# Kernel optimization log

Hardware: AMD Instinct MI355X
Metric: run time of the kernel (lower is better)

The kernel has to match this reference:

```python
import jax, jax.numpy as jnp
import numpy as np

B, N, K, H = 1, 8192, 32, 16
FIBER_IN = (16, 8)
NC_OUT = {'00': 8, '10': 8, '01': 4, '11': 4}
# (pair_key, nc_in, nc_out, num_freq) with num_freq = 2*min(di,do)+1
PAIRS = (('00', 16, 8, 1), ('10', 8, 8, 1), ('01', 16, 4, 1), ('11', 8, 4, 3))


def _silu(x):
    return x * jax.nn.sigmoid(x)


def _ln(x, g):
    mu = x.mean(-1, keepdims=True)
    var = ((x - mu) ** 2).mean(-1, keepdims=True)
    return (x - mu) * jax.lax.rsqrt(var + 1e-5) * g


def _radial(feat, p):
    # Linear -> SiLU -> LayerNorm -> Linear -> SiLU -> LayerNorm -> Linear
    w1, b1, g1, w2, b2, g2, w3, b3 = p
    h = _ln(_silu(feat @ w1 + b1), g1)
    h = _ln(_silu(h @ w2 + b2), g2)
    return h @ w3 + b3


def _lin(x, w):
    # degreewise Linear: einsum('... d m, d e -> ... e m')
    return jnp.einsum('bndm,de->bnem', x, w)


def _forward(x0, x1, rel_dist, bases, w_xi, w_xj, rps, w_out, w_si, nbr_idx, nbr_mask):
    inp = {0: x0, 1: x1}
    xi = {d: _lin(inp[d], w_xi[d]) for d in (0, 1)}
    xj = {d: _lin(inp[d], w_xj[d]) for d in (0, 1)}
    gather = jax.vmap(lambda f, i: f[i])  # per batch: [n,d,m],[n,k] -> [n,k,d,m]
    mask = nbr_mask.astype(x0.dtype)  # [b,n,k]
    denom = jnp.maximum(mask.sum(-1), 1.0)[..., None, None]  # [b,n,1,1]
    b, n, k = nbr_idx.shape
    outs = {}
    for do in (0, 1):
        chunks = []
        for di in (0, 1):
            pkey = str(di) + str(do)
            ci, co = FIBER_IN[di], NC_OUT[pkey]
            nf = 2 * min(di, do) + 1
            xg = gather(xj[di], nbr_idx) + xi[di][:, :, None]  # [b,n,k,ci,mi]
            R = _radial(rel_dist, rps[pkey]).reshape(b, n, k, co, ci, nf)
            Bt = bases[pkey].reshape(b, n, k, 2 * do + 1, 2 * di + 1, nf)  # [b,n,k,mo,mi,nf]
            # kernel = sum_f R[...,o,i,f] * B[...,mo,mi,f]; out = kernel @ x  (done in 2 cheap steps)
            tmp = jnp.einsum('bnkpqf,bnkiq->bnkpfi', Bt, xg)
            chunks.append(jnp.einsum('bnkoif,bnkpfi->bnkop', R, tmp))  # [b,n,k,co,mo]
        out = jnp.concatenate(chunks, axis=3)  # [b,n,k,dim_out,mo]
        outs[do] = (out * mask[..., None, None]).sum(2) / denom  # masked mean over neighbors
    o0 = _lin(outs[0], w_out[0]) + _lin(x0, w_si[0])
    o1 = _lin(outs[1], w_out[1]) + _lin(x1, w_si[1])
    return (o0, o1)


def setup_inputs():
    ks = iter(jax.random.split(jax.random.key(0), 80))
    nrm = lambda shp: jax.random.normal(next(ks), shp, jnp.float32)
    lin_w = lambda i, o: nrm((i, o)) / float(np.sqrt(i))
    d = {}
    d['x0'] = nrm((B, N, 16, 1))
    d['x1'] = nrm((B, N, 8, 3))
    d['rel_dist'] = jax.random.uniform(next(ks), (B, N, K, 1), jnp.float32)
    for nm, ci, co, nf in PAIRS:
        di, do = int(nm[0]), int(nm[1])
        d['basis_' + nm[0] + '_' + nm[1]] = nrm((B, N, K, 1, 2 * do + 1, 1, 2 * di + 1, nf))
    d['w_xi0'] = lin_w(16, 16); d['w_xi1'] = lin_w(8, 8)
    d['w_xj0'] = lin_w(16, 16); d['w_xj1'] = lin_w(8, 8)
    for nm, ci, co, nf in PAIRS:
        d['rp' + nm + '_w1'] = lin_w(1, H)
        d['rp' + nm + '_b1'] = jnp.zeros((H,), jnp.float32)
        d['rp' + nm + '_g1'] = jnp.ones((H,), jnp.float32)
        d['rp' + nm + '_w2'] = lin_w(H, H)
        d['rp' + nm + '_b2'] = jnp.zeros((H,), jnp.float32)
        d['rp' + nm + '_g2'] = jnp.ones((H,), jnp.float32)
        d['rp' + nm + '_w3'] = lin_w(H, nf * ci * co)
        d['rp' + nm + '_b3'] = jnp.zeros((nf * ci * co,), jnp.float32)
    d['w_out0'] = lin_w(16, 16); d['w_out1'] = lin_w(8, 8)
    d['w_si0'] = lin_w(16, 16); d['w_si1'] = lin_w(8, 8)
    d['neighbor_indices'] = jax.random.randint(next(ks), (B, N, K), 0, N, jnp.int32)
    d['neighbor_mask'] = jax.random.randint(next(ks), (B, N, K), 0, 2, jnp.int32).astype(bool)
    return d


def reference(x0, x1, rel_dist, basis_0_0, basis_1_0, basis_0_1, basis_1_1, w_xi0, w_xi1, w_xj0, w_xj1, rp00_w1, rp00_b1, rp00_g1, rp00_w2, rp00_b2, rp00_g2, rp00_w3, rp00_b3, rp10_w1, rp10_b1, rp10_g1, rp10_w2, rp10_b2, rp10_g2, rp10_w3, rp10_b3, rp01_w1, rp01_b1, rp01_g1, rp01_w2, rp01_b2, rp01_g2, rp01_w3, rp01_b3, rp11_w1, rp11_b1, rp11_g1, rp11_w2, rp11_b2, rp11_g2, rp11_w3, rp11_b3, w_out0, w_out1, w_si0, w_si1, neighbor_indices, neighbor_mask):
    bases = {'00': basis_0_0, '10': basis_1_0, '01': basis_0_1, '11': basis_1_1}
    rps = {
        '00': (rp00_w1, rp00_b1, rp00_g1, rp00_w2, rp00_b2, rp00_g2, rp00_w3, rp00_b3),
        '10': (rp10_w1, rp10_b1, rp10_g1, rp10_w2, rp10_b2, rp10_g2, rp10_w3, rp10_b3),
        '01': (rp01_w1, rp01_b1, rp01_g1, rp01_w2, rp01_b2, rp01_g2, rp01_w3, rp01_b3),
        '11': (rp11_w1, rp11_b1, rp11_g1, rp11_w2, rp11_b2, rp11_g2, rp11_w3, rp11_b3),
    }
    return _forward(x0, x1, rel_dist, bases, (w_xi0, w_xi1), (w_xj0, w_xj1), rps, (w_out0, w_out1), (w_si0, w_si1), neighbor_indices, neighbor_mask)
```

## Files before the change

### kernel.cpp

```cpp
#include <hip/hip_runtime.h>


#define NNODE 8192

#define XI0_OFF   0
#define XJ0_OFF   131072
#define XI1_OFF   262144
#define XJ1_OFF   458752
#define INT0_OFF  655360
#define INT1_OFF  786432
#define WTS2_OFF  983040
#define FLAG_OFF  990640

#define RAD00 0
#define RAD01 336
#define RAD10 672
#define RAD11 1008
#define RADN  1344
#define B3_00   1344
#define W3TT_00 1472
#define B3_01   3584
#define W3TT_01 3648
#define B3_10   4736
#define W3TT_10 4800
#define B3F_11  5888
#define W3TT_11 5984
#define BLOB_N  7584

#define YP 72

typedef __attribute__((ext_vector_type(8))) short short8v;
typedef __attribute__((ext_vector_type(4))) float float4v;

static __device__ __forceinline__ float fsilu(float x) {
    return x * (1.0f / (1.0f + __expf(-x)));
}

static __device__ __forceinline__ float dot16(const float* __restrict__ w, const float* h) {
    const float4* w4 = (const float4*)w;
    float4 a = w4[0], b = w4[1], c = w4[2], d = w4[3];
    float s0 = a.x * h[0];  s0 = fmaf(a.y, h[1], s0);  s0 = fmaf(a.z, h[2],  s0);  s0 = fmaf(a.w, h[3],  s0);
    float s1 = b.x * h[4];  s1 = fmaf(b.y, h[5], s1);  s1 = fmaf(b.z, h[6],  s1);  s1 = fmaf(b.w, h[7],  s1);
    float s2 = c.x * h[8];  s2 = fmaf(c.y, h[9], s2);  s2 = fmaf(c.z, h[10], s2);  s2 = fmaf(c.w, h[11], s2);
    float s3 = d.x * h[12]; s3 = fmaf(d.y, h[13], s3); s3 = fmaf(d.z, h[14], s3);  s3 = fmaf(d.w, h[15], s3);
    return (s0 + s1) + (s2 + s3);
}

static __device__ __forceinline__ void ln16ip(float* x, const float* __restrict__ g) {
    float mu = 0.f;
#pragma unroll
    for (int h = 0; h < 16; ++h) mu += x[h];
    mu *= 0.0625f;
    float var = 0.f;
#pragma unroll
    for (int h = 0; h < 16; ++h) { float d = x[h] - mu; var = fmaf(d, d, var); }
    var *= 0.0625f;
    const float s = rsqrtf(var + 1e-5f);
#pragma unroll
    for (int h = 0; h < 16; ++h) x[h] = (x[h] - mu) * s * g[h];
}

static __device__ __forceinline__ void radial16(float dist, const float* __restrict__ w, float* hh) {
    float t[16];
#pragma unroll
    for (int h = 0; h < 16; ++h) t[h] = fsilu(fmaf(dist, w[h], w[16 + h]));
    ln16ip(t, w + 32);
#pragma unroll
    for (int e = 0; e < 16; ++e) hh[e] = fsilu(w[48 + e] + dot16(w + 80 + e * 16, t));
    ln16ip(hh, w + 64);
}

static __device__ __forceinline__ short f2b(float x) {
    unsigned u = __float_as_uint(x);
    u += 0x7FFFu + ((u >> 16) & 1u);
    return (short)(u >> 16);
}

__global__ __launch_bounds__(256) void k_lin_in(
    const float* __restrict__ x0, const float* __restrict__ x1,
    const float* __restrict__ wxi0, const float* __restrict__ wxj0,
    const float* __restrict__ wxi1, const float* __restrict__ wxj1,
    float* __restrict__ xi0, float* __restrict__ xj0,
    float* __restrict__ xi1, float* __restrict__ xj1) {
    const int t = blockIdx.x * 256 + threadIdx.x;
    const int n = t >> 4, e = t & 15;
    const float* xr = x0 + n * 16;
    float si = 0.f, sj = 0.f;
#pragma unroll
    for (int d = 0; d < 16; ++d) {
        const float xv = xr[d];
        si = fmaf(xv, wxi0[d * 16 + e], si);
        sj = fmaf(xv, wxj0[d * 16 + e], sj);
    }
    xi0[t] = si; xj0[t] = sj;
    if (e < 8) {
        const float* x1r = x1 + n * 24;
#pragma unroll
        for (int m = 0; m < 3; ++m) {
            float a = 0.f, b = 0.f;
#pragma unroll
            for (int d = 0; d < 8; ++d) {
                const float xv = x1r[d * 3 + m];
                a = fmaf(xv, wxi1[d * 8 + e], a);
                b = fmaf(xv, wxj1[d * 8 + e], b);
            }
            xi1[n * 24 + e * 3 + m] = a;
            xj1[n * 24 + e * 3 + m] = b;
        }
    }
}

struct RPtrs { const float* a[32]; };

__global__ void k_wts2(RPtrs rp, const unsigned char* __restrict__ maskb,
                       float* __restrict__ wts, int* __restrict__ flagp) {
    const int tid = threadIdx.x;
    const int radO[4] = {RAD00, RAD01, RAD10, RAD11};
    const int rpi[4]  = {0, 2, 1, 3};
#pragma unroll
    for (int pp = 0; pp < 4; ++pp) {
        float* rd = wts + radO[pp];
        const float* w1 = rp.a[rpi[pp] * 8 + 0]; const float* b1 = rp.a[rpi[pp] * 8 + 1];
        const float* g1 = rp.a[rpi[pp] * 8 + 2]; const float* w2 = rp.a[rpi[pp] * 8 + 3];
        const float* b2 = rp.a[rpi[pp] * 8 + 4]; const float* g2 = rp.a[rpi[pp] * 8 + 5];
        if (tid < 16) {
            rd[tid] = w1[tid]; rd[16 + tid] = b1[tid]; rd[32 + tid] = g1[tid];
            rd[48 + tid] = b2[tid]; rd[64 + tid] = g2[tid];
        }
        { const int e = tid >> 4, h = tid & 15; rd[80 + tid] = w2[h * 16 + e]; }
    }
    {
        const float* w3 = rp.a[0 * 8 + 6]; const float* b3 = rp.a[0 * 8 + 7];
        for (int i = tid; i < 128; i += 256) wts[B3_00 + i] = b3[i];
        for (int i = tid; i < 16 * 128; i += 256) {
            const int h = i >> 7, c = i & 127;
            wts[W3TT_00 + h * 132 + c] = w3[i];
        }
    }
    {
        const float* w3 = rp.a[2 * 8 + 6]; const float* b3 = rp.a[2 * 8 + 7];
        for (int i = tid; i < 64; i += 256) wts[B3_01 + i] = b3[i];
        for (int i = tid; i < 16 * 64; i += 256) {
            const int h = i >> 6, c = i & 63;
            wts[W3TT_01 + h * 68 + c] = w3[i];
        }
    }
    {
        const float* w3 = rp.a[1 * 8 + 6]; const float* b3 = rp.a[1 * 8 + 7];
        for (int i = tid; i < 64; i += 256) wts[B3_10 + i] = b3[i];
        for (int i = tid; i < 16 * 64; i += 256) {
            const int h = i >> 6, c = i & 63;
            wts[W3TT_10 + h * 68 + c] = w3[i];
        }
    }
    {
        const float* w3 = rp.a[3 * 8 + 6]; const float* b3 = rp.a[3 * 8 + 7];
        for (int i = tid; i < 96; i += 256) {
            const int c8 = i / 3, f = i % 3;
            wts[B3F_11 + f * 32 + c8] = b3[i];
        }
        for (int i = tid; i < 16 * 96; i += 256) {
            const int h = i / 96, cc = i % 96, c8 = cc / 3, f = cc % 3;
            wts[W3TT_11 + h * 100 + f * 32 + c8] = w3[i];
        }
    }
    if (tid == 0) {
        int nz = 0;
        for (int i = 1; i < 64; ++i) if (i & 3) nz |= (int)maskb[i];
        *flagp = (nz != 0) ? 1 : 0;
    }
}

__global__ __launch_bounds__(256) void k_mfma(
    const float* __restrict__ rel,
    const float* __restrict__ b00, const float* __restrict__ b01,
    const float* __restrict__ b10, const float* __restrict__ b11,
    const int* __restrict__ nbr, const unsigned char* __restrict__ maskb,
    const float* __restrict__ xi0, const float* __restrict__ xj0,
    const float* __restrict__ xi1, const float* __restrict__ xj1,
    const float* __restrict__ wts2, const int* __restrict__ flagp,
    float* __restrict__ o0, float* __restrict__ o1) {
    __shared__ __align__(16) float blobr[RADN];
    __shared__ __align__(16) short ybuf[4][16][YP];
    __shared__ __align__(16) short hbuf[4][16][YP];

    {
        const float4* g4 = (const float4*)wts2;
        float4* s4 = (float4*)blobr;
        for (int i = threadIdx.x; i < RADN / 4; i += 256) s4[i] = g4[i];
    }
    __syncthreads();

    const int w  = threadIdx.x >> 6;
    const int l  = threadIdx.x & 63;
    const int n0 = blockIdx.x * 8 + w * 2;
    const int nl = n0 + (l >> 5);
    const int j  = nl * 32 + (l & 31);

    const int idx = nbr[j];
    const float dist = rel[j];
    const int bytelay = *flagp;
    const int mv = bytelay ? (int)maskb[j] : ((const int*)maskb)[j];
    const float mf = mv ? 1.f : 0.f;

    float cnt = mf;
#pragma unroll
    for (int off = 16; off > 0; off >>= 1) cnt += __shfl_xor(cnt, off);
    const float inv  = 1.f / fmaxf(cnt, 1.f);
    const float invN0 = __shfl(inv, 0);
    const float invN1 = __shfl(inv, 32);

    float xg0[16];
    {
        const float4* a = (const float4*)(xj0 + idx * 16);
        const float4* b = (const float4*)(xi0 + nl * 16);
#pragma unroll
        for (int q = 0; q < 4; ++q) {
            const float4 u = a[q], v = b[q];
            xg0[4 * q + 0] = (u.x + v.x) * mf; xg0[4 * q + 1] = (u.y + v.y) * mf;
            xg0[4 * q + 2] = (u.z + v.z) * mf; xg0[4 * q + 3] = (u.w + v.w) * mf;
        }
    }
    float xg1[8][3];
    {
        const float4* a = (const float4*)(xj1 + idx * 24);
        const float4* b = (const float4*)(xi1 + nl * 24);
        float tmp[24];
#pragma unroll
        for (int q = 0; q < 6; ++q) {
            const float4 u = a[q], v = b[q];
            tmp[4 * q + 0] = (u.x + v.x) * mf; tmp[4 * q + 1] = (u.y + v.y) * mf;
            tmp[4 * q + 2] = (u.z + v.z) * mf; tmp[4 * q + 3] = (u.w + v.w) * mf;
        }
#pragma unroll
        for (int i = 0; i < 8; ++i)
#pragma unroll
            for (int m = 0; m < 3; ++m) xg1[i][m] = tmp[i * 3 + m];
    }

    const int m16 = l & 15;
    const int g4i = l >> 4;
    const int rb  = g4i * 4;
    const int ks  = g4i * 8;
    const bool rv8 = (g4i < 2);
    const bool h0  = (m16 == 0);

    const short one_b = (short)0x3F80;
    const short8v ones = {one_b, one_b, one_b, one_b, one_b, one_b, one_b, one_b};
    const float4v zero4 = {0.f, 0.f, 0.f, 0.f};

    float hh[16];

    {
        radial16(dist, blobr + RAD00, hh);
#pragma unroll
        for (int h = 0; h < 16; ++h) hbuf[w][h][l] = f2b(hh[h]);
        const float Bv = b00[j];
#pragma unroll
        for (int i = 0; i < 16; ++i) ybuf[w][i][l] = f2b(Bv * xg0[i]);

        const float* w3g = wts2 + W3TT_00;
        const float* b3g = wts2 + B3_00;
        float p[2][8];
#pragma unroll
        for (int a = 0; a < 2; ++a)
#pragma unroll
            for (int o = 0; o < 8; ++o) p[a][o] = 0.f;
#pragma unroll
        for (int h2 = 0; h2 < 2; ++h2) {
            const short8v bfr = *(const short8v*)&hbuf[w][m16][ks + h2 * 32];
            const short8v afr = *(const short8v*)&ybuf[w][m16][ks + h2 * 32];
            const float4v V = __builtin_amdgcn_mfma_f32_16x16x32_bf16(afr, bfr, zero4, 0, 0, 0);
            const float4v U = __builtin_amdgcn_mfma_f32_16x16x32_bf16(afr, ones, zero4, 0, 0, 0);
#pragma unroll
            for (int o = 0; o < 8; ++o) {
                const float4 w4 = *(const float4*)&w3g[m16 * 132 + o * 16 + rb];
                p[h2][o] += w4.x * V[0] + w4.y * V[1] + w4.z * V[2] + w4.w * V[3];
                const float4 bb = *(const float4*)&b3g[o * 16 + rb];
                const float du = bb.x * U[0] + bb.y * U[1] + bb.z * U[2] + bb.w * U[3];
                p[h2][o] = h0 ? p[h2][o] + du : p[h2][o];
            }
        }
#pragma unroll
        for (int off = 32; off > 0; off >>= 1)
#pragma unroll
            for (int a = 0; a < 2; ++a)
#pragma unroll
                for (int o = 0; o < 8; ++o) p[a][o] += __shfl_xor(p[a][o], off);
        if (l == 0) {
#pragma unroll
            for (int o = 0; o < 8; ++o) {
                o0[(n0 + 0) * 16 + o] = p[0][o] * invN0;
                o0[(n0 + 1) * 16 + o] = p[1][o] * invN1;
            }
        }
    }

    {
        radial16(dist, blobr + RAD01, hh);
#pragma unroll
        for (int h = 0; h < 16; ++h) hbuf[w][h][l] = f2b(hh[h]);
        const float* bp = b01 + j * 3;
        const float B0 = bp[0], B1 = bp[1], B2 = bp[2];
        const float* w3g = wts2 + W3TT_01;
        const float* b3g = wts2 + B3_01;
        float p[2][4][3];
#pragma unroll
        for (int a = 0; a < 2; ++a)
#pragma unroll
            for (int o = 0; o < 4; ++o)
#pragma unroll
                for (int m = 0; m < 3; ++m) p[a][o][m] = 0.f;
#pragma unroll
        for (int mo = 0; mo < 3; ++mo) {
            const float Bv = (mo == 0) ? B0 : ((mo == 1) ? B1 : B2);
#pragma unroll
            for (int i = 0; i < 16; ++i) ybuf[w][i][l] = f2b(Bv * xg0[i]);
#pragma unroll
            for (int h2 = 0; h2 < 2; ++h2) {
                const short8v bfr = *(const short8v*)&hbuf[w][m16][ks + h2 * 32];
                const short8v afr = *(const short8v*)&ybuf[w][m16][ks + h2 * 32];
                const float4v V = __builtin_amdgcn_mfma_f32_16x16x32_bf16(afr, bfr, zero4, 0, 0, 0);
                const float4v U = __builtin_amdgcn_mfma_f32_16x16x32_bf16(afr, ones, zero4, 0, 0, 0);
#pragma unroll
                for (int o = 0; o < 4; ++o) {
                    const float4 w4 = *(const float4*)&w3g[m16 * 68 + o * 16 + rb];
                    p[h2][o][mo] += w4.x * V[0] + w4.y * V[1] + w4.z * V[2] + w4.w * V[3];
                    const float4 bb = *(const float4*)&b3g[o * 16 + rb];
                    const float du = bb.x * U[0] + bb.y * U[1] + bb.z * U[2] + bb.w * U[3];
                    p[h2][o][mo] = h0 ? p[h2][o][mo] + du : p[h2][o][mo];
                }
            }
        }
#pragma unroll
        for (int off = 32; off > 0; off >>= 1)
#pragma unroll
            for (int a = 0; a < 2; ++a)
#pragma unroll
                for (int o = 0; o < 4; ++o)
#pragma unroll
                    for (int m = 0; m < 3; ++m) p[a][o][m] += __shfl_xor(p[a][o][m], off);
        if (l == 0) {
#pragma unroll
            for (int o = 0; o < 4; ++o)
#pragma unroll
                for (int m = 0; m < 3; ++m) {
                    o1[(n0 + 0) * 24 + o * 3 + m] = p[0][o][m] * invN0;
                    o1[(n0 + 1) * 24 + o * 3 + m] = p[1][o][m] * invN1;
                }
        }
    }

    {
        radial16(dist, blobr + RAD10, hh);
#pragma unroll
        for (int h = 0; h < 16; ++h) hbuf[w][h][l] = f2b(hh[h]);
        const float* bp = b10 + j * 3;
        const float B0 = bp[0], B1 = bp[1], B2 = bp[2];
#pragma unroll
        for (int i = 0; i < 8; ++i)
            ybuf[w][i][l] = f2b(fmaf(B2, xg1[i][2], fmaf(B1, xg1[i][1], B0 * xg1[i][0])));
        const float* w3g = wts2 + W3TT_10;
        const float* b3g = wts2 + B3_10;
        float p[2][8];
#pragma unroll
        for (int a = 0; a < 2; ++a)
#pragma unroll
            for (int o = 0; o < 8; ++o) p[a][o] = 0.f;
#pragma unroll
        for (int h2 = 0; h2 < 2; ++h2) {
            const short8v bfr = *(const short8v*)&hbuf[w][m16][ks + h2 * 32];
            const short8v afr = *(const short8v*)&ybuf[w][m16][ks + h2 * 32];
            const float4v V = __builtin_amdgcn_mfma_f32_16x16x32_bf16(afr, bfr, zero4, 0, 0, 0);
            const float4v U = __builtin_amdgcn_mfma_f32_16x16x32_bf16(afr, ones, zero4, 0, 0, 0);
#pragma unroll
            for (int o = 0; o < 8; ++o) {
                const float4 w4 = *(const float4*)&w3g[m16 * 68 + o * 8 + rb];
                const float dv = w4.x * V[0] + w4.y * V[1] + w4.z * V[2] + w4.w * V[3];
                p[h2][o] = rv8 ? p[h2][o] + dv : p[h2][o];
                const float4 bb = *(const float4*)&b3g[o * 8 + rb];
                const float du = bb.x * U[0] + bb.y * U[1] + bb.z * U[2] + bb.w * U[3];
                p[h2][o] = (rv8 && h0) ? p[h2][o] + du : p[h2][o];
            }
        }
#pragma unroll
        for (int off = 32; off > 0; off >>= 1)
#pragma unroll
            for (int a = 0; a < 2; ++a)
#pragma unroll
                for (int o = 0; o < 8; ++o) p[a][o] += __shfl_xor(p[a][o], off);
        if (l == 0) {
#pragma unroll
            for (int o = 0; o < 8; ++o) {
                o0[(n0 + 0) * 16 + 8 + o] = p[0][o] * invN0;
                o0[(n0 + 1) * 16 + 8 + o] = p[1][o] * invN1;
            }
        }
    }

    {
        radial16(dist, blobr + RAD11, hh);
#pragma unroll
        for (int h = 0; h < 16; ++h) hbuf[w][h][l] = f2b(hh[h]);
        const float* bp = b11 + (size_t)j * 27;
        const float* w3g = wts2 + W3TT_11;
        const float* b3g = wts2 + B3F_11;
        float p[2][4][3];
#pragma unroll
        for (int a = 0; a < 2; ++a)
#pragma unroll
            for (int o = 0; o < 4; ++o)
#pragma unroll
                for (int m = 0; m < 3; ++m) p[a][o][m] = 0.f;
#pragma unroll
        for (int mo = 0; mo < 3; ++mo) {
#pragma unroll
            for (int f = 0; f < 3; ++f) {
                const float c0 = bp[mo * 9 + 0 + f], c1 = bp[mo * 9 + 3 + f], c2 = bp[mo * 9 + 6 + f];
#pragma unroll
                for (int i = 0; i < 8; ++i)
                    ybuf[w][i][l] = f2b(fmaf(c2, xg1[i][2], fmaf(c1, xg1[i][1], c0 * xg1[i][0])));
#pragma unroll
                for (int h2 = 0; h2 < 2; ++h2) {
                    const short8v bfr = *(const short8v*)&hbuf[w][m16][ks + h2 * 32];
                    const short8v afr = *(const short8v*)&ybuf[w][m16][ks + h2 * 32];
                    const float4v V = __builtin_amdgcn_mfma_f32_16x16x32_bf16(afr, bfr, zero4, 0, 0, 0);
                    const float4v U = __builtin_amdgcn_mfma_f32_16x16x32_bf16(afr, ones, zero4, 0, 0, 0);
#pragma unroll
                    for (int o = 0; o < 4; ++o) {
                        const float4 w4 = *(const float4*)&w3g[m16 * 100 + f * 32 + o * 8 + rb];
                        const float dv = w4.x * V[0] + w4.y * V[1] + w4.z * V[2] + w4.w * V[3];
                        p[h2][o][mo] = rv8 ? p[h2][o][mo] + dv : p[h2][o][mo];
                        const float4 bb = *(const float4*)&b3g[f * 32 + o * 8 + rb];
                        const float du = bb.x * U[0] + bb.y * U[1] + bb.z * U[2] + bb.w * U[3];
                        p[h2][o][mo] = (rv8 && h0) ? p[h2][o][mo] + du : p[h2][o][mo];
                    }
                }
            }
        }
#pragma unroll
        for (int off = 32; off > 0; off >>= 1)
#pragma unroll
            for (int a = 0; a < 2; ++a)
#pragma unroll
                for (int o = 0; o < 4; ++o)
#pragma unroll
                    for (int m = 0; m < 3; ++m) p[a][o][m] += __shfl_xor(p[a][o][m], off);
        if (l == 0) {
#pragma unroll
            for (int o = 0; o < 4; ++o)
#pragma unroll
                for (int m = 0; m < 3; ++m) {
                    o1[(n0 + 0) * 24 + (4 + o) * 3 + m] = p[0][o][m] * invN0;
                    o1[(n0 + 1) * 24 + (4 + o) * 3 + m] = p[1][o][m] * invN1;
                }
        }
    }
}

__global__ __launch_bounds__(256) void k_out(
    const float* __restrict__ x0, const float* __restrict__ x1,
    const float* __restrict__ i0, const float* __restrict__ i1,
    const float* __restrict__ wo0, const float* __restrict__ wo1,
    const float* __restrict__ ws0, const float* __restrict__ ws1,
    float* __restrict__ out) {
    const int t = blockIdx.x * 256 + threadIdx.x;
    if (t < 131072) {
        const int n = t >> 4, e = t & 15;
        float s = 0.f;
#pragma unroll
        for (int d = 0; d < 16; ++d) {
            s = fmaf(i0[n * 16 + d], wo0[d * 16 + e], s);
            s = fmaf(x0[n * 16 + d], ws0[d * 16 + e], s);
        }
        out[t] = s;
    } else if (t < 327680) {
        const int u = t - 131072;
        const int n = u / 24, r2 = u % 24, e = r2 / 3, m = r2 % 3;
        float s = 0.f;
#pragma unroll
        for (int d = 0; d < 8; ++d) {
            s = fmaf(i1[n * 24 + d * 3 + m], wo1[d * 8 + e], s);
            s = fmaf(x1[n * 24 + d * 3 + m], ws1[d * 8 + e], s);
        }
        out[t] = s;
    }
}

extern "C" void kernel_launch(void* const* d_in, const int* in_sizes, int n_in,
                              void* d_out, int out_size, void* d_ws, size_t ws_size,
                              hipStream_t stream) {
    const float* x0  = (const float*)d_in[0];
    const float* x1  = (const float*)d_in[1];
    const float* rel = (const float*)d_in[2];
    const float* b00 = (const float*)d_in[3];
    const float* b10 = (const float*)d_in[4];
    const float* b01 = (const float*)d_in[5];
    const float* b11 = (const float*)d_in[6];
    const float* wxi0 = (const float*)d_in[7];
    const float* wxi1 = (const float*)d_in[8];
    const float* wxj0 = (const float*)d_in[9];
    const float* wxj1 = (const float*)d_in[10];
    RPtrs rp;
    for (int i = 0; i < 32; ++i) rp.a[i] = (const float*)d_in[11 + i];
    const float* wo0 = (const float*)d_in[43];
    const float* wo1 = (const float*)d_in[44];
    const float* ws0 = (const float*)d_in[45];
    const float* ws1 = (const float*)d_in[46];
    const int* nbr = (const int*)d_in[47];
    const unsigned char* maskb = (const unsigned char*)d_in[48];

    float* ws = (float*)d_ws;
    float* xi0 = ws + XI0_OFF; float* xj0 = ws + XJ0_OFF;
    float* xi1 = ws + XI1_OFF; float* xj1 = ws + XJ1_OFF;
    float* i0  = ws + INT0_OFF; float* i1 = ws + INT1_OFF;
    float* wts2 = ws + WTS2_OFF;
    int* flagp = (int*)(ws + FLAG_OFF);

    hipLaunchKernelGGL(k_lin_in, dim3(512), dim3(256), 0, stream,
                       x0, x1, wxi0, wxj0, wxi1, wxj1, xi0, xj0, xi1, xj1);
    hipLaunchKernelGGL(k_wts2, dim3(1), dim3(256), 0, stream, rp, maskb, wts2, flagp);
    hipLaunchKernelGGL(k_mfma, dim3(1024), dim3(256), 0, stream,
                       rel, b00, b01, b10, b11, nbr, maskb,
                       xi0, xj0, xi1, xj1, wts2, flagp, i0, i1);
    hipLaunchKernelGGL(k_out, dim3(1280), dim3(256), 0, stream,
                       x0, x1, i0, i1, wo0, wo1, ws0, ws1, (float*)d_out);
}
```

Before: 134.9 us.

## Split degree pairs across warps so each wave handles one pair

Before, each of the four waves in a block processed two nodes through all four degree-pair paths in sequence. Now every wave in a block works on the same two nodes, each wave takes one degree pair (00, 01, 10 or 11), and the grid grows fourfold. This cuts the serial work per wave and the register pressure from holding both xg0 and xg1, which could improve occupancy. The cost is that each block now loads the gather inputs redundantly across waves, and the pairs are unbalanced (pair 11 has far more work), so some waves idle.

```diff
diff --git a/kernel.cpp b/kernel.cpp
--- a/kernel.cpp
+++ b/kernel.cpp
@@ -193,7 +193,7 @@
 
     const int w  = threadIdx.x >> 6;
     const int l  = threadIdx.x & 63;
-    const int n0 = blockIdx.x * 8 + w * 2;
+    const int n0 = blockIdx.x * 2;
     const int nl = n0 + (l >> 5);
     const int j  = nl * 32 + (l & 31);
 
@@ -209,34 +209,6 @@
     const float inv  = 1.f / fmaxf(cnt, 1.f);
     const float invN0 = __shfl(inv, 0);
     const float invN1 = __shfl(inv, 32);
-
-    float xg0[16];
-    {
-        const float4* a = (const float4*)(xj0 + idx * 16);
-        const float4* b = (const float4*)(xi0 + nl * 16);
-#pragma unroll
-        for (int q = 0; q < 4; ++q) {
-            const float4 u = a[q], v = b[q];
-            xg0[4 * q + 0] = (u.x + v.x) * mf; xg0[4 * q + 1] = (u.y + v.y) * mf;
-            xg0[4 * q + 2] = (u.z + v.z) * mf; xg0[4 * q + 3] = (u.w + v.w) * mf;
-        }
-    }
-    float xg1[8][3];
-    {
-        const float4* a = (const float4*)(xj1 + idx * 24);
-        const float4* b = (const float4*)(xi1 + nl * 24);
-        float tmp[24];
-#pragma unroll
-        for (int q = 0; q < 6; ++q) {
-            const float4 u = a[q], v = b[q];
-            tmp[4 * q + 0] = (u.x + v.x) * mf; tmp[4 * q + 1] = (u.y + v.y) * mf;
-            tmp[4 * q + 2] = (u.z + v.z) * mf; tmp[4 * q + 3] = (u.w + v.w) * mf;
-        }
-#pragma unroll
-        for (int i = 0; i < 8; ++i)
-#pragma unroll
-            for (int m = 0; m < 3; ++m) xg1[i][m] = tmp[i * 3 + m];
-    }
 
     const int m16 = l & 15;
     const int g4i = l >> 4;
@@ -250,11 +222,22 @@
     const float4v zero4 = {0.f, 0.f, 0.f, 0.f};
 
     float hh[16];
-
-    {
-        radial16(dist, blobr + RAD00, hh);
-#pragma unroll
-        for (int h = 0; h < 16; ++h) hbuf[w][h][l] = f2b(hh[h]);
+    radial16(dist, blobr + w * 336, hh);
+#pragma unroll
+    for (int h = 0; h < 16; ++h) hbuf[w][h][l] = f2b(hh[h]);
+
+    if (w == 0) {
+        float xg0[16];
+        {
+            const float4* a = (const float4*)(xj0 + idx * 16);
+            const float4* b = (const float4*)(xi0 + nl * 16);
+#pragma unroll
+            for (int q = 0; q < 4; ++q) {
+                const float4 u = a[q], v = b[q];
+                xg0[4 * q + 0] = (u.x + v.x) * mf; xg0[4 * q + 1] = (u.y + v.y) * mf;
+                xg0[4 * q + 2] = (u.z + v.z) * mf; xg0[4 * q + 3] = (u.w + v.w) * mf;
+            }
+        }
         const float Bv = b00[j];
 #pragma unroll
         for (int i = 0; i < 16; ++i) ybuf[w][i][l] = f2b(Bv * xg0[i]);
@@ -294,12 +277,18 @@
                 o0[(n0 + 1) * 16 + o] = p[1][o] * invN1;
             }
         }
-    }
-
-    {
-        radial16(dist, blobr + RAD01, hh);
-#pragma unroll
-        for (int h = 0; h < 16; ++h) hbuf[w][h][l] = f2b(hh[h]);
+    } else if (w == 1) {
+        float xg0[16];
+        {
+            const float4* a = (const float4*)(xj0 + idx * 16);
+            const float4* b = (const float4*)(xi0 + nl * 16);
+#pragma unroll
+            for (int q = 0; q < 4; ++q) {
+                const float4 u = a[q], v = b[q];
+                xg0[4 * q + 0] = (u.x + v.x) * mf; xg0[4 * q + 1] = (u.y + v.y) * mf;
+                xg0[4 * q + 2] = (u.z + v.z) * mf; xg0[4 * q + 3] = (u.w + v.w) * mf;
+            }
+        }
         const float* bp = b01 + j * 3;
         const float B0 = bp[0], B1 = bp[1], B2 = bp[2];
         const float* w3g = wts2 + W3TT_01;
@@ -349,12 +338,23 @@
                     o1[(n0 + 1) * 24 + o * 3 + m] = p[1][o][m] * invN1;
                 }
         }
-    }
-
-    {
-        radial16(dist, blobr + RAD10, hh);
-#pragma unroll
-        for (int h = 0; h < 16; ++h) hbuf[w][h][l] = f2b(hh[h]);
+    } else if (w == 2) {
+        float xg1[8][3];
+        {
+            const float4* a = (const float4*)(xj1 + idx * 24);
+            const float4* b = (const float4*)(xi1 + nl * 24);
+            float tmp[24];
+#pragma unroll
+            for (int q = 0; q < 6; ++q) {
+                const float4 u = a[q], v = b[q];
+                tmp[4 * q + 0] = (u.x + v.x) * mf; tmp[4 * q + 1] = (u.y + v.y) * mf;
+                tmp[4 * q + 2] = (u.z + v.z) * mf; tmp[4 * q + 3] = (u.w + v.w) * mf;
+            }
+#pragma unroll
+            for (int i = 0; i < 8; ++i)
+#pragma unroll
+                for (int m = 0; m < 3; ++m) xg1[i][m] = tmp[i * 3 + m];
+        }
         const float* bp = b10 + j * 3;
         const float B0 = bp[0], B1 = bp[1], B2 = bp[2];
 #pragma unroll
@@ -396,12 +396,23 @@
                 o0[(n0 + 1) * 16 + 8 + o] = p[1][o] * invN1;
             }
         }
-    }
-
-    {
-        radial16(dist, blobr + RAD11, hh);
-#pragma unroll
-        for (int h = 0; h < 16; ++h) hbuf[w][h][l] = f2b(hh[h]);
+    } else {
+        float xg1[8][3];
+        {
+            const float4* a = (const float4*)(xj1 + idx * 24);
+            const float4* b = (const float4*)(xi1 + nl * 24);
+            float tmp[24];
+#pragma unroll
+            for (int q = 0; q < 6; ++q) {
+                const float4 u = a[q], v = b[q];
+                tmp[4 * q + 0] = (u.x + v.x) * mf; tmp[4 * q + 1] = (u.y + v.y) * mf;
+                tmp[4 * q + 2] = (u.z + v.z) * mf; tmp[4 * q + 3] = (u.w + v.w) * mf;
+            }
+#pragma unroll
+            for (int i = 0; i < 8; ++i)
+#pragma unroll
+                for (int m = 0; m < 3; ++m) xg1[i][m] = tmp[i * 3 + m];
+        }
         const float* bp = b11 + (size_t)j * 27;
         const float* w3g = wts2 + W3TT_11;
         const float* b3g = wts2 + B3F_11;
@@ -520,7 +531,7 @@
     hipLaunchKernelGGL(k_lin_in, dim3(512), dim3(256), 0, stream,
                        x0, x1, wxi0, wxj0, wxi1, wxj1, xi0, xj0, xi1, xj1);
     hipLaunchKernelGGL(k_wts2, dim3(1), dim3(256), 0, stream, rp, maskb, wts2, flagp);
-    hipLaunchKernelGGL(k_mfma, dim3(1024), dim3(256), 0, stream,
+    hipLaunchKernelGGL(k_mfma, dim3(4096), dim3(256), 0, stream,
                        rel, b00, b01, b10, b11, nbr, maskb,
                        xi0, xj0, xi1, xj1, wts2, flagp, i0, i1);
     hipLaunchKernelGGL(k_out, dim3(1280), dim3(256), 0, stream,
```

After: 125.3 us. 7.1% less time.
